# Kernel optimization log

Measured on AMD Instinct MI355X. Metric: run time of the kernel, lower is better.

The kernel has to match this reference:

```python
import jax, jax.numpy as jnp
import numpy as np

# einspline cubic B-spline basis matrix (4x4)
BASIS = jnp.array([[-1.0, 3.0, -3.0, 1.0],
                   [ 3.0, -6.0, 0.0, 4.0],
                   [-3.0, 3.0, 3.0, 1.0],
                   [ 1.0, 0.0, 0.0, 0.0]], dtype=jnp.float32) / 6.0


def _build_1d_system_matrix(M: int) -> jnp.ndarray:
    """(M+2, M+2) natural-boundary interpolating B-spline system matrix."""
    delta = 1.0 / (M - 1)
    dinv2 = (1.0 / delta) ** 2
    A = np.zeros((M + 2, M + 2), dtype=np.float32)
    A[0, 0] = dinv2; A[0, 1] = -2.0 * dinv2; A[0, 2] = dinv2
    i = np.arange(1, M + 1)
    A[i, i - 1] = 1.0 / 6.0
    A[i, i] = 2.0 / 3.0
    A[i, i + 1] = 1.0 / 6.0
    A[M + 1, M - 1] = dinv2; A[M + 1, M] = -2.0 * dinv2; A[M + 1, M + 1] = dinv2
    return jnp.asarray(A)


def find_coefs_2d(data: jnp.ndarray) -> jnp.ndarray:
    """data: (C, Mx, My) -> coefs: (C, Mx+2, My+2) via separable solves."""
    C, Mx, My = data.shape
    Ax = _build_1d_system_matrix(Mx)
    Ay = _build_1d_system_matrix(My)
    # solve along x for every (c, y)
    d = jnp.transpose(data, (0, 2, 1)).reshape(-1, Mx)          # (C*My, Mx)
    Bx = jnp.zeros((d.shape[0], Mx + 2), dtype=data.dtype).at[:, 1:Mx + 1].set(d)
    cx = jnp.linalg.solve(Ax, Bx.T).T                           # (C*My, Mx+2)
    cx = jnp.transpose(cx.reshape(C, My, Mx + 2), (0, 2, 1))    # (C, Mx+2, My)
    # solve along y for every (c, x)
    d2 = cx.reshape(-1, My)                                      # (C*(Mx+2), My)
    By = jnp.zeros((d2.shape[0], My + 2), dtype=data.dtype).at[:, 1:My + 1].set(d2)
    coefs = jnp.linalg.solve(Ay, By.T).T.reshape(C, Mx + 2, My + 2)
    return coefs


def _axis_index(un: jnp.ndarray, M: int):
    """Cell index + local fraction with out-of-range extrapolation handling."""
    i = jnp.floor(un).astype(jnp.int32)
    t = un - i.astype(un.dtype)
    low = un < 0
    i = jnp.where(low, 0, i)
    t = jnp.where(low, un, t)
    high = un >= M - 2
    i = jnp.where(high, M - 2, i)
    t = jnp.where(high, un - (M - 2), t)
    return i, t


def interpolate_grid_2d(coefs: jnp.ndarray, u: jnp.ndarray) -> jnp.ndarray:
    """coefs: (C, Mx+2, My+2); u: (B, 2) in [0,1]^2 -> (B, C)."""
    C, Mxp2, Myp2 = coefs.shape
    Mx, My = Mxp2 - 2, Myp2 - 2
    ux_norm = u[:, 0] * (Mx - 1)
    uy_norm = u[:, 1] * (My - 1)
    ix, tx = _axis_index(ux_norm, Mx)
    iy, ty = _axis_index(uy_norm, My)
    ones = jnp.ones_like(tx)
    tx_powers = jnp.stack([tx ** 3, tx ** 2, tx, ones], axis=0)  # (4, B)
    ty_powers = jnp.stack([ty ** 3, ty ** 2, ty, ones], axis=0)  # (4, B)
    basis_x = BASIS @ tx_powers                                   # (4, B)
    basis_y = BASIS @ ty_powers                                   # (4, B)
    offsets = jnp.arange(4, dtype=jnp.int32)
    ix_exp = ix[None, :] + offsets[:, None]                       # (4, B)
    iy_exp = iy[None, :] + offsets[:, None]                       # (4, B)
    # 4x4 neighborhood gather: (C, 4, 4, B)
    control_grid = coefs[:, ix_exp[:, None, :], iy_exp[None, :, :]]
    intermediate = jnp.einsum('cijb,ib->cjb', control_grid, basis_x)
    values = jnp.einsum('cjb,jb->cb', intermediate, basis_y)
    return values.T                                               # (B, C)


def setup_inputs() -> dict:
    key = jax.random.key(0)
    k_u, k_d = jax.random.split(key)
    u = jax.random.uniform(k_u, (2000000, 2), dtype=jnp.float32)
    data = jax.random.normal(k_d, (4, 64, 64), dtype=jnp.float32)
    return {"u": u, "data": data}


def reference(u, data):
    coefs = find_coefs_2d(data)
    return interpolate_grid_2d(coefs, u)
```

## Files before the change

### kernel.cpp

```cpp
#include <hip/hip_runtime.h>
#include <math.h>

#define MX 64
#define NC 4
#define NI 66
#define NINT 62

typedef _Float16 half4  __attribute__((ext_vector_type(4)));
typedef _Float16 half2v __attribute__((ext_vector_type(2)));

struct TC { float m[NINT]; float inv[NINT]; };
constexpr TC make_tc() {
    TC tc{};
    double dp = 2.0/3.0;
    tc.m[0] = 0.0f;
    tc.inv[0] = (float)(1.0/dp);
    for (int j = 1; j < NINT; ++j) {
        double m = (1.0/6.0) / dp;
        tc.m[j] = (float)m;
        dp = 2.0/3.0 - m*(1.0/6.0);
        tc.inv[j] = (float)(1.0/dp);
    }
    return tc;
}
__constant__ constexpr TC g_tc = make_tc();

__global__ __launch_bounds__(256) void solve_fused(const float* __restrict__ data,
                                                   float4* __restrict__ coefsOut)
{
    __shared__ float cxS[NC][NI][65];
    __shared__ half4 chS[NI*NI];
    const int t = threadIdx.x;
    const float a = 1.0f/6.0f;

    {
        const int c = t >> 6, y = t & 63;
        const float* g = data + c*(MX*MX) + y;
        float w[NINT];
        const float d0 = g[0];
        #pragma unroll
        for (int j = 0; j < NINT; ++j) w[j] = g[(j+1)*MX];
        const float dM = g[63*MX];
        w[0]      -= a*d0;
        w[NINT-1] -= a*dM;
        #pragma unroll
        for (int j = 1; j < NINT; ++j) w[j] -= g_tc.m[j]*w[j-1];
        float x = w[NINT-1] * g_tc.inv[NINT-1];
        const float c63 = x;
        cxS[c][63][y] = x;
        #pragma unroll
        for (int j = NINT-2; j >= 0; --j) {
            x = (w[j] - a*x) * g_tc.inv[j];
            cxS[c][j+2][y] = x;
        }
        cxS[c][0][y]  = 2.0f*d0 - x;
        cxS[c][1][y]  = d0;
        cxS[c][64][y] = dM;
        cxS[c][65][y] = 2.0f*dM - c63;
    }
    __syncthreads();

    for (int line = t; line < NC*NI; line += 256) {
        const int c = line / NI;
        const int i = line - c*NI;
        const float* g = &cxS[c][i][0];
        _Float16* o = ((_Float16*)&chS[i*NI]) + c;

        float w[NINT];
        const float d0 = g[0];
        #pragma unroll
        for (int j = 0; j < NINT; ++j) w[j] = g[j+1];
        const float dM = g[63];
        w[0]      -= a*d0;
        w[NINT-1] -= a*dM;
        #pragma unroll
        for (int j = 1; j < NINT; ++j) w[j] -= g_tc.m[j]*w[j-1];
        float x = w[NINT-1] * g_tc.inv[NINT-1];
        const float c63 = x;
        o[63*NC] = (_Float16)x;
        #pragma unroll
        for (int j = NINT-2; j >= 0; --j) {
            x = (w[j] - a*x) * g_tc.inv[j];
            o[(j+2)*NC] = (_Float16)x;
        }
        o[0*NC]  = (_Float16)(2.0f*d0 - x);
        o[1*NC]  = (_Float16)d0;
        o[64*NC] = (_Float16)dM;
        o[65*NC] = (_Float16)(2.0f*dM - c63);
    }
    __syncthreads();

    const float4* src = (const float4*)chS;
    for (int s = t; s < (NI*NI)/2; s += 256) coefsOut[s] = src[s];
}

__device__ __forceinline__ float4 eval_pt(const half4* __restrict__ lds,
                                          float ux, float uy)
{
    const float unx = ux * 63.0f;
    const float uny = uy * 63.0f;

    int ix = (int)unx; ix = ix > 62 ? 62 : ix;
    int iy = (int)uny; iy = iy > 62 ? 62 : iy;
    const float tx = unx - (float)ix;
    const float ty = uny - (float)iy;

    const half2v t = __builtin_bit_cast(half2v, __builtin_amdgcn_cvt_pkrtz(tx, ty));
    const half2v c16  = half2v{(_Float16)(1.0f/6.0f), (_Float16)(1.0f/6.0f)};
    const half2v ch   = half2v{(_Float16)0.5f,  (_Float16)0.5f};
    const half2v cnh  = half2v{(_Float16)-0.5f, (_Float16)-0.5f};
    const half2v cn16 = half2v{(_Float16)(-1.0f/6.0f), (_Float16)(-1.0f/6.0f)};
    const half2v cn1  = half2v{(_Float16)-1.0f, (_Float16)-1.0f};
    const half2v c23  = half2v{(_Float16)(2.0f/3.0f), (_Float16)(2.0f/3.0f)};

    const half2v t2 = t*t;
    half2v b0 = (cn16*t + ch)*t;  b0 = (b0 + cnh)*t + c16;
    half2v b1 = (ch*t + cn1)*t2 + c23;
    half2v b2 = (cnh*t + ch)*t;   b2 = (b2 + ch)*t + c16;
    half2v b3 = c16*(t*t2);

    const half2v by0 = __builtin_shufflevector(b0, b0, 1, 1);
    const half2v by1 = __builtin_shufflevector(b1, b1, 1, 1);
    const half2v by2 = __builtin_shufflevector(b2, b2, 1, 1);
    const half2v by3 = __builtin_shufflevector(b3, b3, 1, 1);
    const half2v bx[4] = {
        __builtin_shufflevector(b0, b0, 0, 0),
        __builtin_shufflevector(b1, b1, 0, 0),
        __builtin_shufflevector(b2, b2, 0, 0),
        __builtin_shufflevector(b3, b3, 0, 0),
    };

    const half4* r = lds + (ix*NI + iy);
    half2v t01, t23;
    #pragma unroll
    for (int ar = 0; ar < 4; ++ar) {
        const half4 c0 = r[ar*NI + 0];
        const half4 c1 = r[ar*NI + 1];
        const half4 c2 = r[ar*NI + 2];
        const half4 c3 = r[ar*NI + 3];
        half2v a01 = c0.lo*by0 + c1.lo*by1 + c2.lo*by2 + c3.lo*by3;
        half2v a23 = c0.hi*by0 + c1.hi*by1 + c2.hi*by2 + c3.hi*by3;
        if (ar == 0) { t01 = a01*bx[0];        t23 = a23*bx[0]; }
        else         { t01 = a01*bx[ar] + t01; t23 = a23*bx[ar] + t23; }
    }
    return make_float4((float)t01.x, (float)t01.y, (float)t23.x, (float)t23.y);
}

__global__ __launch_bounds__(512) void interp(const float4* __restrict__ u2,
                                              const float4* __restrict__ coefs4,
                                              float4* __restrict__ out, int NB)
{
    __shared__ half4 lds[NI*NI];
    float4* l4 = (float4*)lds;
    for (int s = threadIdx.x; s < (NI*NI)/2; s += 512) l4[s] = coefs4[s];
    __syncthreads();

    const int stride = gridDim.x * 512;
    for (int b = blockIdx.x*512 + threadIdx.x; b < NB; b += stride) {
        const float4 uu = u2[b];
        const float4 v0 = eval_pt(lds, uu.x, uu.y);
        const float4 v1 = eval_pt(lds, uu.z, uu.w);
        out[2*b]   = v0;
        out[2*b+1] = v1;
    }
}

extern "C" void kernel_launch(void* const* d_in, const int* in_sizes, int n_in,
                              void* d_out, int out_size, void* d_ws, size_t ws_size,
                              hipStream_t stream)
{
    const float* u    = (const float*)d_in[0];
    const float* data = (const float*)d_in[1];
    const int B  = in_sizes[0] / 2;
    const int NB = B / 2;

    float4* coefsQ = (float4*)d_ws;

    solve_fused<<<1, 256, 0, stream>>>(data, coefsQ);
    interp<<<1024, 512, 0, stream>>>((const float4*)u, (const float4*)coefsQ,
                                     (float4*)d_out, NB);
}
```

Baseline: 87.46 us.

## Fuse spline coefficient solve into interpolation kernel, recomputing per block

Removes the single-block solve kernel and its global-memory handoff. Each interpolation block now solves the separable tridiagonal systems itself in shared memory, two channels at a time to keep the LDS footprint small, and then evaluates its points. This drops one kernel launch and the serial single-block prologue. In exchange, every block repeats the solve, mostly on a subset of threads while the others wait at barriers. The grid is halved to 512 blocks with a 4-waves-per-SIMD launch-bounds hint.

```diff
diff --git a/kernel.cpp b/kernel.cpp
--- a/kernel.cpp
+++ b/kernel.cpp
@@ -24,75 +24,6 @@
     return tc;
 }
 __constant__ constexpr TC g_tc = make_tc();
-
-__global__ __launch_bounds__(256) void solve_fused(const float* __restrict__ data,
-                                                   float4* __restrict__ coefsOut)
-{
-    __shared__ float cxS[NC][NI][65];
-    __shared__ half4 chS[NI*NI];
-    const int t = threadIdx.x;
-    const float a = 1.0f/6.0f;
-
-    {
-        const int c = t >> 6, y = t & 63;
-        const float* g = data + c*(MX*MX) + y;
-        float w[NINT];
-        const float d0 = g[0];
-        #pragma unroll
-        for (int j = 0; j < NINT; ++j) w[j] = g[(j+1)*MX];
-        const float dM = g[63*MX];
-        w[0]      -= a*d0;
-        w[NINT-1] -= a*dM;
-        #pragma unroll
-        for (int j = 1; j < NINT; ++j) w[j] -= g_tc.m[j]*w[j-1];
-        float x = w[NINT-1] * g_tc.inv[NINT-1];
-        const float c63 = x;
-        cxS[c][63][y] = x;
-        #pragma unroll
-        for (int j = NINT-2; j >= 0; --j) {
-            x = (w[j] - a*x) * g_tc.inv[j];
-            cxS[c][j+2][y] = x;
-        }
-        cxS[c][0][y]  = 2.0f*d0 - x;
-        cxS[c][1][y]  = d0;
-        cxS[c][64][y] = dM;
-        cxS[c][65][y] = 2.0f*dM - c63;
-    }
-    __syncthreads();
-
-    for (int line = t; line < NC*NI; line += 256) {
-        const int c = line / NI;
-        const int i = line - c*NI;
-        const float* g = &cxS[c][i][0];
-        _Float16* o = ((_Float16*)&chS[i*NI]) + c;
-
-        float w[NINT];
-        const float d0 = g[0];
-        #pragma unroll
-        for (int j = 0; j < NINT; ++j) w[j] = g[j+1];
-        const float dM = g[63];
-        w[0]      -= a*d0;
-        w[NINT-1] -= a*dM;
-        #pragma unroll
-        for (int j = 1; j < NINT; ++j) w[j] -= g_tc.m[j]*w[j-1];
-        float x = w[NINT-1] * g_tc.inv[NINT-1];
-        const float c63 = x;
-        o[63*NC] = (_Float16)x;
-        #pragma unroll
-        for (int j = NINT-2; j >= 0; --j) {
-            x = (w[j] - a*x) * g_tc.inv[j];
-            o[(j+2)*NC] = (_Float16)x;
-        }
-        o[0*NC]  = (_Float16)(2.0f*d0 - x);
-        o[1*NC]  = (_Float16)d0;
-        o[64*NC] = (_Float16)dM;
-        o[65*NC] = (_Float16)(2.0f*dM - c63);
-    }
-    __syncthreads();
-
-    const float4* src = (const float4*)chS;
-    for (int s = t; s < (NI*NI)/2; s += 256) coefsOut[s] = src[s];
-}
 
 __device__ __forceinline__ float4 eval_pt(const half4* __restrict__ lds,
                                           float ux, float uy)
@@ -146,20 +77,82 @@
     return make_float4((float)t01.x, (float)t01.y, (float)t23.x, (float)t23.y);
 }
 
-__global__ __launch_bounds__(512) void interp(const float4* __restrict__ u2,
-                                              const float4* __restrict__ coefs4,
-                                              float4* __restrict__ out, int NB)
+__global__ __launch_bounds__(512, 4) void fused(const float4* __restrict__ u2,
+                                                const float*  __restrict__ data,
+                                                float4* __restrict__ out, int NB)
 {
-    __shared__ half4 lds[NI*NI];
-    float4* l4 = (float4*)lds;
-    for (int s = threadIdx.x; s < (NI*NI)/2; s += 512) l4[s] = coefs4[s];
-    __syncthreads();
+    __shared__ half4 chS[NI*NI];
+    __shared__ float cxS[2][NI][65];
+    const int t = threadIdx.x;
+    const float a = 1.0f/6.0f;
+
+    #pragma unroll
+    for (int c2 = 0; c2 < 2; ++c2) {
+        if (t < 128) {
+            const int cl = t >> 6, y = t & 63;
+            const int c  = c2*2 + cl;
+            const float* g = data + c*(MX*MX) + y;
+            float w[NINT];
+            const float d0 = g[0];
+            #pragma unroll
+            for (int j = 0; j < NINT; ++j) w[j] = g[(j+1)*MX];
+            const float dM = g[63*MX];
+            w[0]      -= a*d0;
+            w[NINT-1] -= a*dM;
+            #pragma unroll
+            for (int j = 1; j < NINT; ++j) w[j] -= g_tc.m[j]*w[j-1];
+            float x = w[NINT-1] * g_tc.inv[NINT-1];
+            const float c63 = x;
+            cxS[cl][63][y] = x;
+            #pragma unroll
+            for (int j = NINT-2; j >= 0; --j) {
+                x = (w[j] - a*x) * g_tc.inv[j];
+                cxS[cl][j+2][y] = x;
+            }
+            cxS[cl][0][y]  = 2.0f*d0 - x;
+            cxS[cl][1][y]  = d0;
+            cxS[cl][64][y] = dM;
+            cxS[cl][65][y] = 2.0f*dM - c63;
+        }
+        __syncthreads();
+
+        if (t < 2*NI) {
+            const int cl = t / NI;
+            const int i  = t - cl*NI;
+            const int c  = c2*2 + cl;
+            const float* g = &cxS[cl][i][0];
+            _Float16* o = ((_Float16*)&chS[i*NI]) + c;
+
+            float w[NINT];
+            const float d0 = g[0];
+            #pragma unroll
+            for (int j = 0; j < NINT; ++j) w[j] = g[j+1];
+            const float dM = g[63];
+            w[0]      -= a*d0;
+            w[NINT-1] -= a*dM;
+            #pragma unroll
+            for (int j = 1; j < NINT; ++j) w[j] -= g_tc.m[j]*w[j-1];
+            float x = w[NINT-1] * g_tc.inv[NINT-1];
+            const float c63 = x;
+            o[63*NC] = (_Float16)x;
+            #pragma unroll
+            for (int j = NINT-2; j >= 0; --j) {
+                x = (w[j] - a*x) * g_tc.inv[j];
+                o[(j+2)*NC] = (_Float16)x;
+            }
+            o[0*NC]  = (_Float16)(2.0f*d0 - x);
+            o[1*NC]  = (_Float16)d0;
+            o[64*NC] = (_Float16)dM;
+            o[65*NC] = (_Float16)(2.0f*dM - c63);
+        }
+        __syncthreads();
+    }
 
     const int stride = gridDim.x * 512;
-    for (int b = blockIdx.x*512 + threadIdx.x; b < NB; b += stride) {
+    for (int b = blockIdx.x*512 + t; b < NB; b += stride) {
         const float4 uu = u2[b];
-        const float4 v0 = eval_pt(lds, uu.x, uu.y);
-        const float4 v1 = eval_pt(lds, uu.z, uu.w);
+        const float4 v0 = eval_pt(chS, uu.x, uu.y);
+        const float4 v1 = eval_pt(chS, uu.z, uu.w);
         out[2*b]   = v0;
         out[2*b+1] = v1;
     }
@@ -174,9 +167,5 @@
     const int B  = in_sizes[0] / 2;
     const int NB = B / 2;
 
-    float4* coefsQ = (float4*)d_ws;
-
-    solve_fused<<<1, 256, 0, stream>>>(data, coefsQ);
-    interp<<<1024, 512, 0, stream>>>((const float4*)u, (const float4*)coefsQ,
-                                     (float4*)d_out, NB);
+    fused<<<512, 512, 0, stream>>>((const float4*)u, data, (float4*)d_out, NB);
 }
```

Result: no change. 87.12 us (-0.4%).
